# Kernel tuning notes

Hardware: AMD Instinct MI355X
Metric: run time of the kernel (lower is better)

The kernel has to match this reference:

```python
import jax, jax.numpy as jnp
import numpy as np

D_IN, D_SC, DM, DS, NC, T, NS, MD = 1536, 234, 64, 8, 234, 12, 20, 8
B = 4096
LN_EPS = 1e-5


def setup_inputs() -> dict:
    key = jax.random.key(0)
    ks = jax.random.split(key, 16)
    r = lambda k, s: (jax.random.normal(k, s, jnp.float32) * 0.02)
    a_log = jnp.log(jnp.tile(jnp.arange(1, DS + 1, dtype=jnp.float32), (DM, 1)))  # (DM, DS)
    return {
        "emb": jax.random.normal(ks[0], (B, T, D_IN), jnp.float32),
        "scores": jax.random.uniform(ks[1], (B, T, D_SC), jnp.float32),
        "site_ids": jax.random.randint(ks[2], (B,), 0, NS),
        "hours": jax.random.randint(ks[3], (B,), 0, 24),
        "W_in": r(ks[4], (D_IN + D_SC, DM)), "b_in": jnp.zeros((DM,), jnp.float32),
        "ln_in_g": jnp.ones((DM,), jnp.float32), "ln_in_b": jnp.zeros((DM,), jnp.float32),
        "site_emb": r(ks[5], (NS, MD)), "hour_emb": r(ks[6], (24, MD)),
        "W_meta": r(ks[7], (2 * MD, DM)), "b_meta": jnp.zeros((DM,), jnp.float32),
        "pos_enc": r(ks[8], (1, T, DM)),
        "A_log_f": a_log, "Wp_f": r(ks[9], (DM, DM + 2 * DS)),
        "bp_f": jnp.zeros((DM + 2 * DS,), jnp.float32), "D_f": jnp.ones((DM,), jnp.float32),
        "A_log_b": a_log, "Wp_b": r(ks[10], (DM, DM + 2 * DS)),
        "bp_b": jnp.zeros((DM + 2 * DS,), jnp.float32), "D_b": jnp.ones((DM,), jnp.float32),
        "W_merge": r(ks[11], (2 * DM, DM)), "b_merge": jnp.zeros((DM,), jnp.float32),
        "ln_g": jnp.ones((DM,), jnp.float32), "ln_b": jnp.zeros((DM,), jnp.float32),
        "W_out": r(ks[12], (DM, NC)), "b_out": jnp.zeros((NC,), jnp.float32),
    }


def _ln(x, g, b):
    mu = x.mean(-1, keepdims=True)
    var = ((x - mu) ** 2).mean(-1, keepdims=True)
    return (x - mu) * jax.lax.rsqrt(var + LN_EPS) * g + b


def _selective_ssm(x, A_log, Wp, bp, D):
    # x: (B, T, DM); Mamba-style selective scan with ZOH discretization.
    proj = x @ Wp + bp                                # (B, T, DM+2*DS)
    delta = jax.nn.softplus(proj[..., :DM])           # (B, T, DM)
    Bc = proj[..., DM:DM + DS]                        # (B, T, DS)
    Cc = proj[..., DM + DS:]                          # (B, T, DS)
    A = -jnp.exp(A_log)                               # (DM, DS)
    dA = jnp.exp(delta[..., None] * A)                # (B, T, DM, DS)
    dBx = (delta * x)[..., None] * Bc[:, :, None, :]  # (B, T, DM, DS)

    def step(h, inp):
        dA_t, dBx_t, C_t = inp
        h = dA_t * h + dBx_t                          # (B, DM, DS)
        y = jnp.einsum('bdn,bn->bd', h, C_t)          # (B, DM)
        return h, y

    h0 = jnp.zeros((x.shape[0], DM, DS), x.dtype)
    _, ys = jax.lax.scan(step, h0, (dA.transpose(1, 0, 2, 3), dBx.transpose(1, 0, 2, 3), Cc.transpose(1, 0, 2)))
    return ys.transpose(1, 0, 2) + x * D              # (B, T, DM)


def reference(emb, scores, site_ids, hours, W_in, b_in, ln_in_g, ln_in_b, site_emb, hour_emb,
              W_meta, b_meta, pos_enc, A_log_f, Wp_f, bp_f, D_f, A_log_b, Wp_b, bp_b, D_b,
              W_merge, b_merge, ln_g, ln_b, W_out, b_out):
    x = jnp.concatenate([emb, scores], axis=-1)       # (B, T, D_IN+D_SC)
    h = jax.nn.gelu(_ln(x @ W_in + b_in, ln_in_g, ln_in_b), approximate=False)
    site_e = site_emb[jnp.clip(site_ids, 0, NS - 1)]  # (B, MD)
    hour_e = hour_emb[jnp.clip(hours, 0, 23)]         # (B, MD)
    meta = jnp.concatenate([site_e, hour_e], axis=-1) @ W_meta + b_meta
    h = h + meta[:, None, :] + pos_enc[:, :T, :]
    residual = h
    h_f = _selective_ssm(h, A_log_f, Wp_f, bp_f, D_f)
    h_b = _selective_ssm(h[:, ::-1, :], A_log_b, Wp_b, bp_b, D_b)[:, ::-1, :]
    h = jnp.concatenate([h_f, h_b], axis=-1) @ W_merge + b_merge
    h = _ln(h + residual, ln_g, ln_b)
    return h @ W_out + b_out                          # (B, T, NC)
```

## Files before the change

kernel.cpp:

```cpp
#include <hip/hip_runtime.h>
#include <hip/hip_bf16.h>

#define D_IN_ 1536
#define D_SC_ 234
#define DM_   64
#define DSN_  8
#define NC_   234
#define T_    12
#define NS_   20
#define B_    4096
#define NROW_ (B_ * T_)
#define KPAD_ 1792
#define LN_EPS_ 1e-5f

typedef __bf16 bf16x8 __attribute__((ext_vector_type(8)));
typedef float  f32x4  __attribute__((ext_vector_type(4)));

__global__ void prep_w(const float* __restrict__ W_in, unsigned short* __restrict__ Wt) {
    int idx = blockIdx.x * 256 + threadIdx.x;
    if (idx >= 64 * KPAD_) return;
    int n = idx / KPAD_, k = idx - n * KPAD_;
    float v = (k < (D_IN_ + D_SC_)) ? W_in[k * 64 + n] : 0.0f;
    __hip_bfloat16 hb = __float2bfloat16(v);
    Wt[idx] = *reinterpret_cast<unsigned short*>(&hb);
}

__global__ void prep_meta(const int* __restrict__ site_ids, const int* __restrict__ hours,
                          const float* __restrict__ site_emb, const float* __restrict__ hour_emb,
                          const float* __restrict__ W_meta, const float* __restrict__ b_meta,
                          float* __restrict__ meta) {
    int idx = blockIdx.x * 256 + threadIdx.x;
    if (idx >= B_ * 64) return;
    int b = idx >> 6, n = idx & 63;
    int s = min(max(site_ids[b], 0), NS_ - 1);
    int h = min(max(hours[b], 0), 23);
    float acc = b_meta[n];
#pragma unroll
    for (int k = 0; k < 8; k++) acc += site_emb[s * 8 + k] * W_meta[k * 64 + n];
#pragma unroll
    for (int k = 0; k < 8; k++) acc += hour_emb[h * 8 + k] * W_meta[(8 + k) * 64 + n];
    meta[idx] = acc;
}

__launch_bounds__(256)
__global__ void k1_gemm(const float* __restrict__ emb, const float* __restrict__ scores,
                        const unsigned short* __restrict__ Wt,
                        const float* __restrict__ b_in, const float* __restrict__ ln_in_g,
                        const float* __restrict__ ln_in_b, const float* __restrict__ meta,
                        const float* __restrict__ pos_enc, float* __restrict__ h_out) {
    __shared__ __align__(16) unsigned short As[64 * 72];
    __shared__ __align__(16) unsigned short Bs[64 * 72];

    const int tid  = threadIdx.x;
    const int lane = tid & 63;
    const int w    = tid >> 6;
    const int q    = lane >> 4;
    const int mm   = lane & 15;
    const int row0 = blockIdx.x * 64;

    f32x4 acc[4];
#pragma unroll
    for (int nt = 0; nt < 4; nt++) acc[nt] = (f32x4){0.f, 0.f, 0.f, 0.f};

    for (int kt = 0; kt < 28; kt++) {
#pragma unroll
        for (int it = 0; it < 2; it++) {
            int i = tid + it * 256;
            int n = i >> 3, c = i & 7;
            const uint4* src = reinterpret_cast<const uint4*>(Wt + n * KPAD_ + kt * 64 + c * 8);
            *reinterpret_cast<uint4*>(&Bs[n * 72 + c * 8]) = *src;
        }
#pragma unroll
        for (int it = 0; it < 2; it++) {
            int i = tid + it * 256;
            int m = i >> 3, c = i & 7;
            int row = row0 + m;
            float v[8];
            if (kt < 24) {
                const float4* s0 = reinterpret_cast<const float4*>(emb + (size_t)row * D_IN_ + kt * 64 + c * 8);
                float4 va = s0[0], vb = s0[1];
                v[0]=va.x; v[1]=va.y; v[2]=va.z; v[3]=va.w;
                v[4]=vb.x; v[5]=vb.y; v[6]=vb.z; v[7]=vb.w;
            } else {
                int kl = (kt - 24) * 64 + c * 8;
#pragma unroll
                for (int j = 0; j < 8; j++) {
                    int k2 = kl + j;
                    v[j] = (k2 < D_SC_) ? scores[(size_t)row * D_SC_ + k2] : 0.0f;
                }
            }
            __hip_bfloat16 bv[8];
#pragma unroll
            for (int j = 0; j < 8; j++) bv[j] = __float2bfloat16(v[j]);
            *reinterpret_cast<uint4*>(&As[m * 72 + c * 8]) = *reinterpret_cast<const uint4*>(bv);
        }
        __syncthreads();
#pragma unroll
        for (int ks = 0; ks < 2; ks++) {
            bf16x8 af = *reinterpret_cast<const bf16x8*>(&As[(w * 16 + mm) * 72 + ks * 32 + q * 8]);
#pragma unroll
            for (int nt = 0; nt < 4; nt++) {
                bf16x8 bfv = *reinterpret_cast<const bf16x8*>(&Bs[(nt * 16 + mm) * 72 + ks * 32 + q * 8]);
                acc[nt] = __builtin_amdgcn_mfma_f32_16x16x32_bf16(af, bfv, acc[nt], 0, 0, 0);
            }
        }
        __syncthreads();
    }

    float binv[4], gl[4], bl[4];
#pragma unroll
    for (int nt = 0; nt < 4; nt++) {
        binv[nt] = b_in[nt * 16 + mm];
        gl[nt]   = ln_in_g[nt * 16 + mm];
        bl[nt]   = ln_in_b[nt * 16 + mm];
    }
#pragma unroll
    for (int nt = 0; nt < 4; nt++)
#pragma unroll
        for (int reg = 0; reg < 4; reg++) acc[nt][reg] += binv[nt];

    float sum[4], sq[4];
#pragma unroll
    for (int reg = 0; reg < 4; reg++) {
        sum[reg] = acc[0][reg] + acc[1][reg] + acc[2][reg] + acc[3][reg];
        sq[reg]  = acc[0][reg]*acc[0][reg] + acc[1][reg]*acc[1][reg]
                 + acc[2][reg]*acc[2][reg] + acc[3][reg]*acc[3][reg];
    }
#pragma unroll
    for (int m2 = 1; m2 <= 8; m2 <<= 1) {
#pragma unroll
        for (int reg = 0; reg < 4; reg++) {
            sum[reg] += __shfl_xor(sum[reg], m2);
            sq[reg]  += __shfl_xor(sq[reg], m2);
        }
    }
#pragma unroll
    for (int reg = 0; reg < 4; reg++) {
        float mu   = sum[reg] * 0.015625f;
        float var  = sq[reg] * 0.015625f - mu * mu;
        float rstd = rsqrtf(var + LN_EPS_);
        int row  = row0 + w * 16 + q * 4 + reg;
        int bidx = row / 12;
        int t    = row - bidx * 12;
        const float* mrow = meta + (size_t)bidx * 64;
        const float* prow = pos_enc + t * 64;
#pragma unroll
        for (int nt = 0; nt < 4; nt++) {
            int n = nt * 16 + mm;
            float x  = (acc[nt][reg] - mu) * rstd * gl[nt] + bl[nt];
            float ge = 0.5f * x * (1.0f + erff(x * 0.70710678118654752f));
            h_out[(size_t)row * 64 + n] = ge + mrow[n] + prow[n];
        }
    }
}

__launch_bounds__(256)
__global__ void k2_ssm(const float* __restrict__ h_in,
                       const float* __restrict__ A_log_f, const float* __restrict__ Wp_f,
                       const float* __restrict__ bp_f, const float* __restrict__ D_f,
                       const float* __restrict__ A_log_b, const float* __restrict__ Wp_b,
                       const float* __restrict__ bp_b, const float* __restrict__ D_b,
                       const float* __restrict__ W_merge, const float* __restrict__ b_merge,
                       const float* __restrict__ ln_g, const float* __restrict__ ln_b,
                       const float* __restrict__ W_out, const float* __restrict__ b_out,
                       float* __restrict__ out) {
    __shared__ __align__(16) float h_s[T_ * 64];
    __shared__ __align__(16) float proj_s[2 * T_ * 80];
    __shared__ __align__(16) float y_s[2 * T_ * 64];
    __shared__ __align__(16) float g_s[T_ * 64];

    const int tid = threadIdx.x;
    const int b   = blockIdx.x;
    const float* hb = h_in + (size_t)b * T_ * 64;

    if (tid < 192)
        reinterpret_cast<float4*>(h_s)[tid] = reinterpret_cast<const float4*>(hb)[tid];
    __syncthreads();

    if (tid < 160) {
        int dir = tid / 80, j = tid - dir * 80;
        const float* Wp = dir ? Wp_b : Wp_f;
        const float* bp = dir ? bp_b : bp_f;
        float acc[T_];
#pragma unroll
        for (int t = 0; t < T_; t++) acc[t] = bp[j];
        for (int kq = 0; kq < 16; kq++) {
            float w0 = Wp[(kq * 4 + 0) * 80 + j];
            float w1 = Wp[(kq * 4 + 1) * 80 + j];
            float w2 = Wp[(kq * 4 + 2) * 80 + j];
            float w3 = Wp[(kq * 4 + 3) * 80 + j];
#pragma unroll
            for (int t = 0; t < T_; t++) {
                int ts = dir ? (T_ - 1 - t) : t;
                float4 hv = *reinterpret_cast<const float4*>(&h_s[ts * 64 + kq * 4]);
                acc[t] += hv.x * w0 + hv.y * w1 + hv.z * w2 + hv.w * w3;
            }
        }
#pragma unroll
        for (int t = 0; t < T_; t++) proj_s[dir * T_ * 80 + t * 80 + j] = acc[t];
    }
    __syncthreads();

    if (tid < 128) {
        int dir = tid >> 6, d = tid & 63;
        const float* Alog = dir ? A_log_b : A_log_f;
        const float* Dp   = dir ? D_b : D_f;
        float4 a0 = *reinterpret_cast<const float4*>(Alog + d * 8);
        float4 a1 = *reinterpret_cast<const float4*>(Alog + d * 8 + 4);
        float a[8];
        a[0] = -__expf(a0.x); a[1] = -__expf(a0.y); a[2] = -__expf(a0.z); a[3] = -__expf(a0.w);
        a[4] = -__expf(a1.x); a[5] = -__expf(a1.y); a[6] = -__expf(a1.z); a[7] = -__expf(a1.w);
        float Dd = Dp[d];
        float st[8];
#pragma unroll
        for (int n = 0; n < 8; n++) st[n] = 0.0f;
        const float* ps = proj_s + dir * T_ * 80;
        for (int t = 0; t < T_; t++) {
            int ts = dir ? (T_ - 1 - t) : t;
            float x    = h_s[ts * 64 + d];
            float draw = ps[t * 80 + d];
            float delta = (draw > 20.0f) ? draw : log1pf(__expf(draw));
            float4 Bc0 = *reinterpret_cast<const float4*>(&ps[t * 80 + 64]);
            float4 Bc1 = *reinterpret_cast<const float4*>(&ps[t * 80 + 68]);
            float4 Cc0 = *reinterpret_cast<const float4*>(&ps[t * 80 + 72]);
            float4 Cc1 = *reinterpret_cast<const float4*>(&ps[t * 80 + 76]);
            float Bv[8] = {Bc0.x, Bc0.y, Bc0.z, Bc0.w, Bc1.x, Bc1.y, Bc1.z, Bc1.w};
            float Cv[8] = {Cc0.x, Cc0.y, Cc0.z, Cc0.w, Cc1.x, Cc1.y, Cc1.z, Cc1.w};
            float dx = delta * x;
            float y = 0.0f;
#pragma unroll
            for (int n = 0; n < 8; n++) {
                st[n] = __expf(delta * a[n]) * st[n] + dx * Bv[n];
                y += st[n] * Cv[n];
            }
            y_s[dir * T_ * 64 + t * 64 + d] = y + x * Dd;
        }
    }
    __syncthreads();

    {
        int j = tid & 63, tg = tid >> 6;
        float accm[3];
#pragma unroll
        for (int i = 0; i < 3; i++) accm[i] = b_merge[j];
        for (int kq = 0; kq < 32; kq++) {
            float w0 = W_merge[(kq * 4 + 0) * 64 + j];
            float w1 = W_merge[(kq * 4 + 1) * 64 + j];
            float w2 = W_merge[(kq * 4 + 2) * 64 + j];
            float w3 = W_merge[(kq * 4 + 3) * 64 + j];
#pragma unroll
            for (int i = 0; i < 3; i++) {
                int t = tg + i * 4;
                float4 yv;
                if (kq < 16) yv = *reinterpret_cast<const float4*>(&y_s[t * 64 + kq * 4]);
                else         yv = *reinterpret_cast<const float4*>(&y_s[T_ * 64 + (T_ - 1 - t) * 64 + (kq - 16) * 4]);
                accm[i] += yv.x * w0 + yv.y * w1 + yv.z * w2 + yv.w * w3;
            }
        }
#pragma unroll
        for (int i = 0; i < 3; i++) {
            int t = tg + i * 4;
            float r  = accm[i] + h_s[t * 64 + j];
            float s1 = r, s2 = r * r;
#pragma unroll
            for (int m2 = 1; m2 < 64; m2 <<= 1) { s1 += __shfl_xor(s1, m2); s2 += __shfl_xor(s2, m2); }
            float mu   = s1 * 0.015625f;
            float var  = s2 * 0.015625f - mu * mu;
            float rstd = rsqrtf(var + LN_EPS_);
            g_s[t * 64 + j] = (r - mu) * rstd * ln_g[j] + ln_b[j];
        }
    }
    __syncthreads();

    if (tid < NC_) {
        int j = tid;
        float acco[T_];
#pragma unroll
        for (int t = 0; t < T_; t++) acco[t] = b_out[j];
        for (int kq = 0; kq < 16; kq++) {
            float w0 = W_out[(kq * 4 + 0) * NC_ + j];
            float w1 = W_out[(kq * 4 + 1) * NC_ + j];
            float w2 = W_out[(kq * 4 + 2) * NC_ + j];
            float w3 = W_out[(kq * 4 + 3) * NC_ + j];
#pragma unroll
            for (int t = 0; t < T_; t++) {
                float4 gv = *reinterpret_cast<const float4*>(&g_s[t * 64 + kq * 4]);
                acco[t] += gv.x * w0 + gv.y * w1 + gv.z * w2 + gv.w * w3;
            }
        }
        float* ob = out + (size_t)b * T_ * NC_;
#pragma unroll
        for (int t = 0; t < T_; t++) ob[t * NC_ + j] = acco[t];
    }
}

extern "C" void kernel_launch(void* const* d_in, const int* in_sizes, int n_in,
                              void* d_out, int out_size, void* d_ws, size_t ws_size,
                              hipStream_t stream) {
    const float* emb      = (const float*)d_in[0];
    const float* scores   = (const float*)d_in[1];
    const int*   site_ids = (const int*)d_in[2];
    const int*   hours    = (const int*)d_in[3];
    const float* W_in     = (const float*)d_in[4];
    const float* b_in     = (const float*)d_in[5];
    const float* ln_in_g  = (const float*)d_in[6];
    const float* ln_in_b  = (const float*)d_in[7];
    const float* site_emb = (const float*)d_in[8];
    const float* hour_emb = (const float*)d_in[9];
    const float* W_meta   = (const float*)d_in[10];
    const float* b_meta   = (const float*)d_in[11];
    const float* pos_enc  = (const float*)d_in[12];
    const float* A_log_f  = (const float*)d_in[13];
    const float* Wp_f     = (const float*)d_in[14];
    const float* bp_f     = (const float*)d_in[15];
    const float* D_f      = (const float*)d_in[16];
    const float* A_log_b  = (const float*)d_in[17];
    const float* Wp_b     = (const float*)d_in[18];
    const float* bp_b     = (const float*)d_in[19];
    const float* D_b      = (const float*)d_in[20];
    const float* W_merge  = (const float*)d_in[21];
    const float* b_merge  = (const float*)d_in[22];
    const float* ln_g     = (const float*)d_in[23];
    const float* ln_b     = (const float*)d_in[24];
    const float* W_out    = (const float*)d_in[25];
    const float* b_out    = (const float*)d_in[26];

    char* ws = (char*)d_ws;
    unsigned short* Wt = (unsigned short*)ws;
    float* meta = (float*)(ws + 229376);
    float* h_ws = (float*)(ws + 229376 + 1048576);

    prep_w   <<<(64 * KPAD_ + 255) / 256, 256, 0, stream>>>(W_in, Wt);
    prep_meta<<<(B_ * 64 + 255) / 256, 256, 0, stream>>>(site_ids, hours, site_emb, hour_emb,
                                                         W_meta, b_meta, meta);
    k1_gemm  <<<NROW_ / 64, 256, 0, stream>>>(emb, scores, Wt, b_in, ln_in_g, ln_in_b,
                                              meta, pos_enc, h_ws);
    k2_ssm   <<<B_, 256, 0, stream>>>(h_ws, A_log_f, Wp_f, bp_f, D_f,
                                      A_log_b, Wp_b, bp_b, D_b,
                                      W_merge, b_merge, ln_g, ln_b, W_out, b_out,
                                      (float*)d_out);
}
```

Measured before the change: 629.7 us.

## Pre-swizzle weights to MFMA fragment layout and use MFMA for SSM-stage GEMMs

The input GEMM no longer stages tiles in shared memory. Each wave owns a 16-row strip and reads pre-swizzled bf16 weight fragments directly from global memory, with register double-buffering of the activation loads. In the SSM kernel, the projection, merge and output GEMMs move from scalar FP32 loops to bf16 MFMA, with operands written into fragment layout in shared memory. The meta vectors are stored as bf16. This removes LDS staging and barriers in k1 and scalar FMA work in k2, at the cost of extra bf16 rounding in the downstream GEMMs and meta.

Result: faster. 562.1 us (-10.7%).

```diff
diff --git a/kernel.cpp b/kernel.cpp
--- a/kernel.cpp
+++ b/kernel.cpp
@@ -4,31 +4,68 @@
 #define D_IN_ 1536
 #define D_SC_ 234
 #define DM_   64
-#define DSN_  8
 #define NC_   234
 #define T_    12
 #define NS_   20
 #define B_    4096
 #define NROW_ (B_ * T_)
-#define KPAD_ 1792
 #define LN_EPS_ 1e-5f
+#define PJS 164
+#define RS_ 68
 
 typedef __bf16 bf16x8 __attribute__((ext_vector_type(8)));
 typedef float  f32x4  __attribute__((ext_vector_type(4)));
 
+static __device__ __forceinline__ unsigned short f2bs(float f) {
+    __hip_bfloat16 h = __float2bfloat16(f);
+    return *reinterpret_cast<unsigned short*>(&h);
+}
+static __device__ __forceinline__ float bs2f(unsigned short u) {
+    __hip_bfloat16 h = *reinterpret_cast<__hip_bfloat16*>(&u);
+    return __bfloat162float(h);
+}
+
 __global__ void prep_w(const float* __restrict__ W_in, unsigned short* __restrict__ Wt) {
     int idx = blockIdx.x * 256 + threadIdx.x;
-    if (idx >= 64 * KPAD_) return;
-    int n = idx / KPAD_, k = idx - n * KPAD_;
+    if (idx >= 28 * 4096) return;
+    int j = idx & 7, ln = (idx >> 3) & 63, nt = (idx >> 9) & 3, ks = (idx >> 11) & 1, kt = idx >> 12;
+    int q = ln >> 4, mm = ln & 15;
+    int n = nt * 16 + mm;
+    int k = kt * 64 + ks * 32 + q * 8 + j;
     float v = (k < (D_IN_ + D_SC_)) ? W_in[k * 64 + n] : 0.0f;
-    __hip_bfloat16 hb = __float2bfloat16(v);
-    Wt[idx] = *reinterpret_cast<unsigned short*>(&hb);
+    Wt[idx] = f2bs(v);
+}
+
+__global__ void prep_small(const float* __restrict__ Wp_f, const float* __restrict__ Wp_b,
+                           const float* __restrict__ W_merge, const float* __restrict__ W_out,
+                           unsigned short* __restrict__ Wpt, unsigned short* __restrict__ Wmt,
+                           unsigned short* __restrict__ Wot) {
+    int idx = blockIdx.x * 256 + threadIdx.x;
+    if (idx >= 33792) return;
+    int j = idx & 7, ln = (idx >> 3) & 63;
+    int q = ln >> 4, mm = ln & 15;
+    if (idx < 10240) {
+        int tile = idx >> 9, nt = tile >> 1, ks = tile & 1;
+        int n = nt * 16 + mm, k = ks * 32 + q * 8 + j;
+        float v = (n >= 80) ? Wp_b[k * 80 + (n - 80)] : Wp_f[k * 80 + n];
+        Wpt[idx] = f2bs(v);
+    } else if (idx < 18432) {
+        int i2 = idx - 10240;
+        int tile = i2 >> 9, nt = tile >> 2, ks = tile & 3;
+        int n = nt * 16 + mm, k = ks * 32 + q * 8 + j;
+        Wmt[i2] = f2bs(W_merge[k * 64 + n]);
+    } else {
+        int i2 = idx - 18432;
+        int tile = i2 >> 9, nt = tile >> 1, ks = tile & 1;
+        int n = nt * 16 + mm, k = ks * 32 + q * 8 + j;
+        Wot[i2] = f2bs((n < NC_) ? W_out[k * NC_ + n] : 0.0f);
+    }
 }
 
 __global__ void prep_meta(const int* __restrict__ site_ids, const int* __restrict__ hours,
                           const float* __restrict__ site_emb, const float* __restrict__ hour_emb,
                           const float* __restrict__ W_meta, const float* __restrict__ b_meta,
-                          float* __restrict__ meta) {
+                          unsigned short* __restrict__ meta_bf) {
     int idx = blockIdx.x * 256 + threadIdx.x;
     if (idx >= B_ * 64) return;
     int b = idx >> 6, n = idx & 63;
@@ -39,72 +76,111 @@
     for (int k = 0; k < 8; k++) acc += site_emb[s * 8 + k] * W_meta[k * 64 + n];
 #pragma unroll
     for (int k = 0; k < 8; k++) acc += hour_emb[h * 8 + k] * W_meta[(8 + k) * 64 + n];
-    meta[idx] = acc;
+    meta_bf[idx] = f2bs(acc);
 }
 
 __launch_bounds__(256)
 __global__ void k1_gemm(const float* __restrict__ emb, const float* __restrict__ scores,
                         const unsigned short* __restrict__ Wt,
                         const float* __restrict__ b_in, const float* __restrict__ ln_in_g,
-                        const float* __restrict__ ln_in_b, const float* __restrict__ meta,
+                        const float* __restrict__ ln_in_b, const unsigned short* __restrict__ meta_bf,
                         const float* __restrict__ pos_enc, float* __restrict__ h_out) {
-    __shared__ __align__(16) unsigned short As[64 * 72];
-    __shared__ __align__(16) unsigned short Bs[64 * 72];
-
     const int tid  = threadIdx.x;
     const int lane = tid & 63;
     const int w    = tid >> 6;
     const int q    = lane >> 4;
     const int mm   = lane & 15;
-    const int row0 = blockIdx.x * 64;
+    const int strip = blockIdx.x * 4 + w;
+    const int row0  = strip * 16;
+
+    const float* aptr = emb + (size_t)(row0 + mm) * D_IN_ + q * 8;
+    const unsigned short* wptr = Wt + lane * 8;
 
     f32x4 acc[4];
 #pragma unroll
     for (int nt = 0; nt < 4; nt++) acc[nt] = (f32x4){0.f, 0.f, 0.f, 0.f};
 
-    for (int kt = 0; kt < 28; kt++) {
-#pragma unroll
-        for (int it = 0; it < 2; it++) {
-            int i = tid + it * 256;
-            int n = i >> 3, c = i & 7;
-            const uint4* src = reinterpret_cast<const uint4*>(Wt + n * KPAD_ + kt * 64 + c * 8);
-            *reinterpret_cast<uint4*>(&Bs[n * 72 + c * 8]) = *src;
-        }
-#pragma unroll
-        for (int it = 0; it < 2; it++) {
-            int i = tid + it * 256;
-            int m = i >> 3, c = i & 7;
-            int row = row0 + m;
-            float v[8];
-            if (kt < 24) {
-                const float4* s0 = reinterpret_cast<const float4*>(emb + (size_t)row * D_IN_ + kt * 64 + c * 8);
-                float4 va = s0[0], vb = s0[1];
-                v[0]=va.x; v[1]=va.y; v[2]=va.z; v[3]=va.w;
-                v[4]=vb.x; v[5]=vb.y; v[6]=vb.z; v[7]=vb.w;
-            } else {
-                int kl = (kt - 24) * 64 + c * 8;
-#pragma unroll
-                for (int j = 0; j < 8; j++) {
-                    int k2 = kl + j;
-                    v[j] = (k2 < D_SC_) ? scores[(size_t)row * D_SC_ + k2] : 0.0f;
+    float4 cur[4];
+#pragma unroll
+    for (int h = 0; h < 4; h++)
+        cur[h] = *reinterpret_cast<const float4*>(aptr + (h >> 1) * 32 + (h & 1) * 4);
+
+    __align__(16) unsigned short av[2][8];
+
+    for (int kt = 0; kt < 23; kt++) {
+        float4 nxt[4];
+#pragma unroll
+        for (int h = 0; h < 4; h++)
+            nxt[h] = *reinterpret_cast<const float4*>(aptr + (kt + 1) * 64 + (h >> 1) * 32 + (h & 1) * 4);
+        bf16x8 bfr[2][4];
+#pragma unroll
+        for (int ks = 0; ks < 2; ks++)
+#pragma unroll
+            for (int nt = 0; nt < 4; nt++)
+                bfr[ks][nt] = *reinterpret_cast<const bf16x8*>(wptr + kt * 4096 + ks * 2048 + nt * 512);
+#pragma unroll
+        for (int ks = 0; ks < 2; ks++) {
+            const float* cf = reinterpret_cast<const float*>(&cur[ks * 2]);
+#pragma unroll
+            for (int j = 0; j < 8; j++) av[ks][j] = f2bs(cf[j]);
+        }
+#pragma unroll
+        for (int ks = 0; ks < 2; ks++) {
+            bf16x8 af = *reinterpret_cast<const bf16x8*>(av[ks]);
+#pragma unroll
+            for (int nt = 0; nt < 4; nt++)
+                acc[nt] = __builtin_amdgcn_mfma_f32_16x16x32_bf16(af, bfr[ks][nt], acc[nt], 0, 0, 0);
+        }
+#pragma unroll
+        for (int h = 0; h < 4; h++) cur[h] = nxt[h];
+    }
+    {
+        const int kt = 23;
+        bf16x8 bfr[2][4];
+#pragma unroll
+        for (int ks = 0; ks < 2; ks++)
+#pragma unroll
+            for (int nt = 0; nt < 4; nt++)
+                bfr[ks][nt] = *reinterpret_cast<const bf16x8*>(wptr + kt * 4096 + ks * 2048 + nt * 512);
+#pragma unroll
+        for (int ks = 0; ks < 2; ks++) {
+            const float* cf = reinterpret_cast<const float*>(&cur[ks * 2]);
+#pragma unroll
+            for (int j = 0; j < 8; j++) av[ks][j] = f2bs(cf[j]);
+        }
+#pragma unroll
+        for (int ks = 0; ks < 2; ks++) {
+            bf16x8 af = *reinterpret_cast<const bf16x8*>(av[ks]);
+#pragma unroll
+            for (int nt = 0; nt < 4; nt++)
+                acc[nt] = __builtin_amdgcn_mfma_f32_16x16x32_bf16(af, bfr[ks][nt], acc[nt], 0, 0, 0);
+        }
+    }
+    {
+        const float* sp = scores + (size_t)(row0 + mm) * D_SC_;
+#pragma unroll
+        for (int kt2 = 0; kt2 < 4; kt2++) {
+#pragma unroll
+            for (int ks = 0; ks < 2; ks++) {
+                int c0 = kt2 * 64 + ks * 32 + q * 8;
+                __align__(16) unsigned short avt[8];
+#pragma unroll
+                for (int p = 0; p < 4; p++) {
+                    int c = c0 + 2 * p;
+                    float2 v;
+                    if (c + 1 < D_SC_) v = *reinterpret_cast<const float2*>(sp + c);
+                    else { v.x = 0.0f; v.y = 0.0f; }
+                    avt[2 * p]     = f2bs(v.x);
+                    avt[2 * p + 1] = f2bs(v.y);
+                }
+                bf16x8 af = *reinterpret_cast<const bf16x8*>(avt);
+#pragma unroll
+                for (int nt = 0; nt < 4; nt++) {
+                    bf16x8 bv = *reinterpret_cast<const bf16x8*>(wptr + (24 + kt2) * 4096 + ks * 2048 + nt * 512);
+                    acc[nt] = __builtin_amdgcn_mfma_f32_16x16x32_bf16(af, bv, acc[nt], 0, 0, 0);
                 }
             }
-            __hip_bfloat16 bv[8];
-#pragma unroll
-            for (int j = 0; j < 8; j++) bv[j] = __float2bfloat16(v[j]);
-            *reinterpret_cast<uint4*>(&As[m * 72 + c * 8]) = *reinterpret_cast<const uint4*>(bv);
-        }
-        __syncthreads();
-#pragma unroll
-        for (int ks = 0; ks < 2; ks++) {
-            bf16x8 af = *reinterpret_cast<const bf16x8*>(&As[(w * 16 + mm) * 72 + ks * 32 + q * 8]);
-#pragma unroll
-            for (int nt = 0; nt < 4; nt++) {
-                bf16x8 bfv = *reinterpret_cast<const bf16x8*>(&Bs[(nt * 16 + mm) * 72 + ks * 32 + q * 8]);
-                acc[nt] = __builtin_amdgcn_mfma_f32_16x16x32_bf16(af, bfv, acc[nt], 0, 0, 0);
-            }
-        }
-        __syncthreads();
+        }
     }
 
     float binv[4], gl[4], bl[4];
@@ -139,65 +215,79 @@
         float mu   = sum[reg] * 0.015625f;
         float var  = sq[reg] * 0.015625f - mu * mu;
         float rstd = rsqrtf(var + LN_EPS_);
-        int row  = row0 + w * 16 + q * 4 + reg;
+        int row  = row0 + q * 4 + reg;
         int bidx = row / 12;
         int t    = row - bidx * 12;
-        const float* mrow = meta + (size_t)bidx * 64;
+        const unsigned short* mrow = meta_bf + (size_t)bidx * 64;
         const float* prow = pos_enc + t * 64;
 #pragma unroll
         for (int nt = 0; nt < 4; nt++) {
             int n = nt * 16 + mm;
             float x  = (acc[nt][reg] - mu) * rstd * gl[nt] + bl[nt];
             float ge = 0.5f * x * (1.0f + erff(x * 0.70710678118654752f));
-            h_out[(size_t)row * 64 + n] = ge + mrow[n] + prow[n];
+            h_out[(size_t)row * 64 + n] = ge + bs2f(mrow[n]) + prow[n];
         }
     }
 }
 
 __launch_bounds__(256)
 __global__ void k2_ssm(const float* __restrict__ h_in,
-                       const float* __restrict__ A_log_f, const float* __restrict__ Wp_f,
-                       const float* __restrict__ bp_f, const float* __restrict__ D_f,
-                       const float* __restrict__ A_log_b, const float* __restrict__ Wp_b,
-                       const float* __restrict__ bp_b, const float* __restrict__ D_b,
-                       const float* __restrict__ W_merge, const float* __restrict__ b_merge,
-                       const float* __restrict__ ln_g, const float* __restrict__ ln_b,
-                       const float* __restrict__ W_out, const float* __restrict__ b_out,
+                       const float* __restrict__ A_log_f, const float* __restrict__ bp_f,
+                       const float* __restrict__ D_f,
+                       const float* __restrict__ A_log_b, const float* __restrict__ bp_b,
+                       const float* __restrict__ D_b,
+                       const unsigned short* __restrict__ Wpt, const unsigned short* __restrict__ Wmt,
+                       const unsigned short* __restrict__ Wot,
+                       const float* __restrict__ b_merge, const float* __restrict__ ln_g,
+                       const float* __restrict__ ln_b, const float* __restrict__ b_out,
                        float* __restrict__ out) {
-    __shared__ __align__(16) float h_s[T_ * 64];
-    __shared__ __align__(16) float proj_s[2 * T_ * 80];
-    __shared__ __align__(16) float y_s[2 * T_ * 64];
-    __shared__ __align__(16) float g_s[T_ * 64];
-
-    const int tid = threadIdx.x;
-    const int b   = blockIdx.x;
-    const float* hb = h_in + (size_t)b * T_ * 64;
-
-    if (tid < 192)
-        reinterpret_cast<float4*>(h_s)[tid] = reinterpret_cast<const float4*>(hb)[tid];
+    __shared__ float h_s[T_ * 64];
+    __shared__ __align__(16) unsigned short hb_s[1024];
+    __shared__ float proj_s[T_ * PJS];
+    __shared__ __align__(16) unsigned short yb_s[2048];
+    __shared__ float r_s[T_ * RS_];
+    __shared__ __align__(16) unsigned short gb_s[1024];
+
+    const int tid  = threadIdx.x;
+    const int lane = tid & 63;
+    const int w    = tid >> 6;
+    const int q    = lane >> 4;
+    const int mm   = lane & 15;
+    const int b    = blockIdx.x;
+
+    if (tid < 192) {
+        float4 hv = reinterpret_cast<const float4*>(h_in + (size_t)b * (T_ * 64))[tid];
+        *reinterpret_cast<float4*>(&h_s[tid * 4]) = hv;
+        int m = tid >> 4, c0 = (tid & 15) * 4;
+        int base = (c0 >> 5) * 512 + (((c0 >> 3) & 3) * 16 + m) * 8 + (c0 & 7);
+        hb_s[base + 0] = f2bs(hv.x);
+        hb_s[base + 1] = f2bs(hv.y);
+        hb_s[base + 2] = f2bs(hv.z);
+        hb_s[base + 3] = f2bs(hv.w);
+    }
     __syncthreads();
 
-    if (tid < 160) {
-        int dir = tid / 80, j = tid - dir * 80;
-        const float* Wp = dir ? Wp_b : Wp_f;
-        const float* bp = dir ? bp_b : bp_f;
-        float acc[T_];
-#pragma unroll
-        for (int t = 0; t < T_; t++) acc[t] = bp[j];
-        for (int kq = 0; kq < 16; kq++) {
-            float w0 = Wp[(kq * 4 + 0) * 80 + j];
-            float w1 = Wp[(kq * 4 + 1) * 80 + j];
-            float w2 = Wp[(kq * 4 + 2) * 80 + j];
-            float w3 = Wp[(kq * 4 + 3) * 80 + j];
-#pragma unroll
-            for (int t = 0; t < T_; t++) {
-                int ts = dir ? (T_ - 1 - t) : t;
-                float4 hv = *reinterpret_cast<const float4*>(&h_s[ts * 64 + kq * 4]);
-                acc[t] += hv.x * w0 + hv.y * w1 + hv.z * w2 + hv.w * w3;
+    {
+        bf16x8 a0 = *reinterpret_cast<const bf16x8*>(&hb_s[lane * 8]);
+        bf16x8 a1 = *reinterpret_cast<const bf16x8*>(&hb_s[512 + lane * 8]);
+#pragma unroll
+        for (int i = 0; i < 3; i++) {
+            int nt = w + i * 4;
+            if (nt < 10) {
+                bf16x8 b0 = *reinterpret_cast<const bf16x8*>(Wpt + (nt * 2 + 0) * 512 + lane * 8);
+                bf16x8 b1 = *reinterpret_cast<const bf16x8*>(Wpt + (nt * 2 + 1) * 512 + lane * 8);
+                f32x4 c = (f32x4){0.f, 0.f, 0.f, 0.f};
+                c = __builtin_amdgcn_mfma_f32_16x16x32_bf16(a0, b0, c, 0, 0, 0);
+                c = __builtin_amdgcn_mfma_f32_16x16x32_bf16(a1, b1, c, 0, 0, 0);
+                int n = nt * 16 + mm;
+                float bpv = (n >= 80) ? bp_b[n - 80] : bp_f[n];
+                if (q < 3) {
+#pragma unroll
+                    for (int reg = 0; reg < 4; reg++)
+                        proj_s[(q * 4 + reg) * PJS + n] = c[reg] + bpv;
+                }
             }
         }
-#pragma unroll
-        for (int t = 0; t < T_; t++) proj_s[dir * T_ * 80 + t * 80 + j] = acc[t];
     }
     __syncthreads();
 
@@ -205,27 +295,25 @@
         int dir = tid >> 6, d = tid & 63;
         const float* Alog = dir ? A_log_b : A_log_f;
         const float* Dp   = dir ? D_b : D_f;
-        float4 a0 = *reinterpret_cast<const float4*>(Alog + d * 8);
-        float4 a1 = *reinterpret_cast<const float4*>(Alog + d * 8 + 4);
         float a[8];
-        a[0] = -__expf(a0.x); a[1] = -__expf(a0.y); a[2] = -__expf(a0.z); a[3] = -__expf(a0.w);
-        a[4] = -__expf(a1.x); a[5] = -__expf(a1.y); a[6] = -__expf(a1.z); a[7] = -__expf(a1.w);
+#pragma unroll
+        for (int n = 0; n < 8; n++) a[n] = -__expf(Alog[d * 8 + n]);
         float Dd = Dp[d];
         float st[8];
 #pragma unroll
         for (int n = 0; n < 8; n++) st[n] = 0.0f;
-        const float* ps = proj_s + dir * T_ * 80;
         for (int t = 0; t < T_; t++) {
             int ts = dir ? (T_ - 1 - t) : t;
             float x    = h_s[ts * 64 + d];
-            float draw = ps[t * 80 + d];
+            float draw = proj_s[ts * PJS + dir * 80 + d];
             float delta = (draw > 20.0f) ? draw : log1pf(__expf(draw));
-            float4 Bc0 = *reinterpret_cast<const float4*>(&ps[t * 80 + 64]);
-            float4 Bc1 = *reinterpret_cast<const float4*>(&ps[t * 80 + 68]);
-            float4 Cc0 = *reinterpret_cast<const float4*>(&ps[t * 80 + 72]);
-            float4 Cc1 = *reinterpret_cast<const float4*>(&ps[t * 80 + 76]);
-            float Bv[8] = {Bc0.x, Bc0.y, Bc0.z, Bc0.w, Bc1.x, Bc1.y, Bc1.z, Bc1.w};
-            float Cv[8] = {Cc0.x, Cc0.y, Cc0.z, Cc0.w, Cc1.x, Cc1.y, Cc1.z, Cc1.w};
+            const float* pb = &proj_s[ts * PJS + dir * 80 + 64];
+            float4 B0 = *reinterpret_cast<const float4*>(pb);
+            float4 B1 = *reinterpret_cast<const float4*>(pb + 4);
+            float4 C0 = *reinterpret_cast<const float4*>(pb + 8);
+            float4 C1 = *reinterpret_cast<const float4*>(pb + 12);
+            float Bv[8] = {B0.x, B0.y, B0.z, B0.w, B1.x, B1.y, B1.z, B1.w};
+            float Cv[8] = {C0.x, C0.y, C0.z, C0.w, C1.x, C1.y, C1.z, C1.w};
             float dx = delta * x;
             float y = 0.0f;
 #pragma unroll
@@ -233,64 +321,77 @@
                 st[n] = __expf(delta * a[n]) * st[n] + dx * Bv[n];
                 y += st[n] * Cv[n];
             }
-            y_s[dir * T_ * 64 + t * 64 + d] = y + x * Dd;
+            float yv = y + x * Dd;
+            int kk = dir * 64 + d;
+            yb_s[(kk >> 5) * 512 + (((kk >> 3) & 3) * 16 + ts) * 8 + (kk & 7)] = f2bs(yv);
         }
     }
     __syncthreads();
 
     {
-        int j = tid & 63, tg = tid >> 6;
-        float accm[3];
-#pragma unroll
-        for (int i = 0; i < 3; i++) accm[i] = b_merge[j];
-        for (int kq = 0; kq < 32; kq++) {
-            float w0 = W_merge[(kq * 4 + 0) * 64 + j];
-            float w1 = W_merge[(kq * 4 + 1) * 64 + j];
-            float w2 = W_merge[(kq * 4 + 2) * 64 + j];
-            float w3 = W_merge[(kq * 4 + 3) * 64 + j];
-#pragma unroll
-            for (int i = 0; i < 3; i++) {
-                int t = tg + i * 4;
-                float4 yv;
-                if (kq < 16) yv = *reinterpret_cast<const float4*>(&y_s[t * 64 + kq * 4]);
-                else         yv = *reinterpret_cast<const float4*>(&y_s[T_ * 64 + (T_ - 1 - t) * 64 + (kq - 16) * 4]);
-                accm[i] += yv.x * w0 + yv.y * w1 + yv.z * w2 + yv.w * w3;
+        int nt = w;
+        f32x4 c = (f32x4){0.f, 0.f, 0.f, 0.f};
+#pragma unroll
+        for (int ks = 0; ks < 4; ks++) {
+            bf16x8 A = *reinterpret_cast<const bf16x8*>(&yb_s[ks * 512 + lane * 8]);
+            bf16x8 Bm = *reinterpret_cast<const bf16x8*>(Wmt + (nt * 4 + ks) * 512 + lane * 8);
+            c = __builtin_amdgcn_mfma_f32_16x16x32_bf16(A, Bm, c, 0, 0, 0);
+        }
+        int n = nt * 16 + mm;
+        float bm = b_merge[n];
+        if (q < 3) {
+#pragma unroll
+            for (int reg = 0; reg < 4; reg++) {
+                int t = q * 4 + reg;
+                r_s[t * RS_ + n] = c[reg] + bm + h_s[t * 64 + n];
             }
         }
+    }
+    __syncthreads();
+
+    {
+        int j = lane;
 #pragma unroll
         for (int i = 0; i < 3; i++) {
-            int t = tg + i * 4;
-            float r  = accm[i] + h_s[t * 64 + j];
+            int t = w + i * 4;
+            float r  = r_s[t * RS_ + j];
             float s1 = r, s2 = r * r;
 #pragma unroll
             for (int m2 = 1; m2 < 64; m2 <<= 1) { s1 += __shfl_xor(s1, m2); s2 += __shfl_xor(s2, m2); }
             float mu   = s1 * 0.015625f;
             float var  = s2 * 0.015625f - mu * mu;
             float rstd = rsqrtf(var + LN_EPS_);
-            g_s[t * 64 + j] = (r - mu) * rstd * ln_g[j] + ln_b[j];
+            float g = (r - mu) * rstd * ln_g[j] + ln_b[j];
+            gb_s[(j >> 5) * 512 + (((j >> 3) & 3) * 16 + t) * 8 + (j & 7)] = f2bs(g);
         }
     }
     __syncthreads();
 
-    if (tid < NC_) {
-        int j = tid;
-        float acco[T_];
-#pragma unroll
-        for (int t = 0; t < T_; t++) acco[t] = b_out[j];
-        for (int kq = 0; kq < 16; kq++) {
-            float w0 = W_out[(kq * 4 + 0) * NC_ + j];
-            float w1 = W_out[(kq * 4 + 1) * NC_ + j];
-            float w2 = W_out[(kq * 4 + 2) * NC_ + j];
-            float w3 = W_out[(kq * 4 + 3) * NC_ + j];
-#pragma unroll
-            for (int t = 0; t < T_; t++) {
-                float4 gv = *reinterpret_cast<const float4*>(&g_s[t * 64 + kq * 4]);
-                acco[t] += gv.x * w0 + gv.y * w1 + gv.z * w2 + gv.w * w3;
+    {
+        bf16x8 a0 = *reinterpret_cast<const bf16x8*>(&gb_s[lane * 8]);
+        bf16x8 a1 = *reinterpret_cast<const bf16x8*>(&gb_s[512 + lane * 8]);
+#pragma unroll
+        for (int i = 0; i < 4; i++) {
+            int nt = w + i * 4;
+            if (nt < 15) {
+                bf16x8 b0 = *reinterpret_cast<const bf16x8*>(Wot + (nt * 2 + 0) * 512 + lane * 8);
+                bf16x8 b1 = *reinterpret_cast<const bf16x8*>(Wot + (nt * 2 + 1) * 512 + lane * 8);
+                f32x4 c = (f32x4){0.f, 0.f, 0.f, 0.f};
+                c = __builtin_amdgcn_mfma_f32_16x16x32_bf16(a0, b0, c, 0, 0, 0);
+                c = __builtin_amdgcn_mfma_f32_16x16x32_bf16(a1, b1, c, 0, 0, 0);
+                int n = nt * 16 + mm;
+                if (n < NC_) {
+                    float bo = b_out[n];
+                    if (q < 3) {
+#pragma unroll
+                        for (int reg = 0; reg < 4; reg++) {
+                            int t = q * 4 + reg;
+                            out[(size_t)b * (T_ * NC_) + t * NC_ + n] = c[reg] + bo;
+                        }
+                    }
+                }
             }
         }
-        float* ob = out + (size_t)b * T_ * NC_;
-#pragma unroll
-        for (int t = 0; t < T_; t++) ob[t * NC_ + j] = acco[t];
     }
 }
 
@@ -326,17 +427,18 @@
     const float* b_out    = (const float*)d_in[26];
 
     char* ws = (char*)d_ws;
-    unsigned short* Wt = (unsigned short*)ws;
-    float* meta = (float*)(ws + 229376);
-    float* h_ws = (float*)(ws + 229376 + 1048576);
-
-    prep_w   <<<(64 * KPAD_ + 255) / 256, 256, 0, stream>>>(W_in, Wt);
-    prep_meta<<<(B_ * 64 + 255) / 256, 256, 0, stream>>>(site_ids, hours, site_emb, hour_emb,
-                                                         W_meta, b_meta, meta);
-    k1_gemm  <<<NROW_ / 64, 256, 0, stream>>>(emb, scores, Wt, b_in, ln_in_g, ln_in_b,
-                                              meta, pos_enc, h_ws);
-    k2_ssm   <<<B_, 256, 0, stream>>>(h_ws, A_log_f, Wp_f, bp_f, D_f,
-                                      A_log_b, Wp_b, bp_b, D_b,
-                                      W_merge, b_merge, ln_g, ln_b, W_out, b_out,
-                                      (float*)d_out);
-}
+    unsigned short* Wt      = (unsigned short*)(ws + 0);
+    unsigned short* meta_bf = (unsigned short*)(ws + 229376);
+    unsigned short* Wpt     = (unsigned short*)(ws + 753664);
+    unsigned short* Wmt     = (unsigned short*)(ws + 774144);
+    unsigned short* Wot     = (unsigned short*)(ws + 790528);
+    float*          h_ws    = (float*)(ws + 821248);
+
+    prep_w      <<<448, 256, 0, stream>>>(W_in, Wt);
+    prep_small  <<<132, 256, 0, stream>>>(Wp_f, Wp_b, W_merge, W_out, Wpt, Wmt, Wot);
+    prep_meta   <<<1024, 256, 0, stream>>>(site_ids, hours, site_emb, hour_emb, W_meta, b_meta, meta_bf);
+    k1_gemm     <<<768, 256, 0, stream>>>(emb, scores, Wt, b_in, ln_in_g, ln_in_b, meta_bf, pos_enc, h_ws);
+    k2_ssm      <<<4096, 256, 0, stream>>>(h_ws, A_log_f, bp_f, D_f, A_log_b, bp_b, D_b,
+                                           Wpt, Wmt, Wot, b_merge, ln_g, ln_b, b_out,
+                                           (float*)d_out);
+}
```
